# Optimization experiments

Hardware: AMD Instinct MI355X
Metric: run time of the kernel (lower is better)

## Reference

```python
import jax, jax.numpy as jnp
import numpy as np

B, N, M, D, H = 2, 512, 512, 128, 256
EPS = 1e-5


def _layernorm(x, g, b):
    mu = jnp.mean(x, axis=-1, keepdims=True)
    var = jnp.mean(jnp.square(x - mu), axis=-1, keepdims=True)
    return (x - mu) * jax.lax.rsqrt(var + EPS) * g + b


def setup_inputs() -> dict:
    key = jax.random.key(0)
    ks = jax.random.split(key, 12)
    X = jax.random.normal(ks[0], (B, N, D), dtype=jnp.float32)
    Y = jax.random.normal(ks[1], (B, M, D), dtype=jnp.float32)
    mask = jax.random.randint(ks[2], (B, N, M), 0, 2).astype(jnp.int32)
    s_in = 1.0 / np.sqrt(2 * D)
    s_h = 1.0 / np.sqrt(H)
    s_d = 1.0 / np.sqrt(D)
    # edge-net Linear(2D, H) split into Y-half and X-half (pairs = cat([Y, X]))
    W1y = jax.random.normal(ks[3], (D, H), dtype=jnp.float32) * s_in
    W1x = jax.random.normal(ks[4], (D, H), dtype=jnp.float32) * s_in
    b1 = jnp.zeros((H,), dtype=jnp.float32)
    W2 = jax.random.normal(ks[5], (H, D), dtype=jnp.float32) * s_h
    b2 = jnp.zeros((D,), dtype=jnp.float32)
    Wf1 = jax.random.normal(ks[6], (D, H), dtype=jnp.float32) * s_d
    bf1 = jnp.zeros((H,), dtype=jnp.float32)
    Wf2 = jax.random.normal(ks[7], (H, D), dtype=jnp.float32) * s_h
    bf2 = jnp.zeros((D,), dtype=jnp.float32)
    g0 = jnp.ones((D,), dtype=jnp.float32)
    be0 = jnp.zeros((D,), dtype=jnp.float32)
    g1 = jnp.ones((D,), dtype=jnp.float32)
    be1 = jnp.zeros((D,), dtype=jnp.float32)
    return {"X": X, "Y": Y, "mask": mask, "W1y": W1y, "W1x": W1x, "b1": b1,
            "W2": W2, "b2": b2, "Wf1": Wf1, "bf1": bf1, "Wf2": Wf2, "bf2": bf2,
            "g0": g0, "be0": be0, "g1": g1, "be1": be1}


def reference(X, Y, mask, W1y, W1x, b1, W2, b2, Wf1, bf1, Wf2, bf2, g0, be0, g1, be1):
    # pairs[b,n,m] = concat(Y[b,m], X[b,n]); Linear on concat == sum of two GEMMs,
    # so avoid materializing the [B,N,M,2D] pairs tensor.
    hy = jnp.einsum('bmd,dh->bmh', Y, W1y)          # [B,M,H]
    hx = jnp.einsum('bnd,dh->bnh', X, W1x)          # [B,N,H]
    h = jax.nn.relu(hy[:, None, :, :] + hx[:, :, None, :] + b1)   # [B,N,M,H]
    E = jnp.einsum('bnmh,hd->bnmd', h, W2) + b2     # [B,N,M,D]
    E = E * mask[..., None].astype(E.dtype)         # masked sum-pool over M
    Z = X + jnp.sum(E, axis=2)                      # residual, [B,N,D]
    Z = _layernorm(Z, g0, be0)
    Z = Z + jax.nn.relu(Z @ Wf1 + bf1) @ Wf2 + bf2  # residual MLP
    Z = _layernorm(Z, g1, be1)
    return Z
```

## Files before the change

kernel.cpp:

```cpp
#include <hip/hip_runtime.h>

#define BB 2
#define NN 512
#define MM 512
#define DD 128
#define HH 256

__global__ __launch_bounds__(256) void k_inproj(
    const float* __restrict__ X, const float* __restrict__ Y,
    const float* __restrict__ W1x, const float* __restrict__ W1y,
    const float* __restrict__ b1,
    float* __restrict__ hx, float* __restrict__ hy)
{
    __shared__ float sr[DD][4];
    int blk = blockIdx.x;
    bool isX = blk < 256;
    const float* src = isX ? X : Y;
    const float* W   = isX ? W1x : W1y;
    float* dst       = isX ? hx : hy;
    int row0 = (isX ? blk : blk - 256) * 4;
    int t = threadIdx.x;

#pragma unroll
    for (int k = 0; k < 2; ++k) {
        int idx = t + k * 256;
        int r = idx >> 7, d = idx & 127;
        sr[d][r] = src[(row0 + r) * DD + d];
    }
    __syncthreads();

    float bias = isX ? b1[t] : 0.0f;
    float a0 = bias, a1 = bias, a2 = bias, a3 = bias;

#pragma unroll 16
    for (int d = 0; d < DD; ++d) {
        float w = W[d * HH + t];
        float4 a = *(const float4*)&sr[d][0];
        a0 = fmaf(a.x, w, a0);
        a1 = fmaf(a.y, w, a1);
        a2 = fmaf(a.z, w, a2);
        a3 = fmaf(a.w, w, a3);
    }
    dst[(row0 + 0) * HH + t] = a0;
    dst[(row0 + 1) * HH + t] = a1;
    dst[(row0 + 2) * HH + t] = a2;
    dst[(row0 + 3) * HH + t] = a3;
}

__global__ __launch_bounds__(256) void k_main(
    const float* __restrict__ hx, const float* __restrict__ hy,
    const int* __restrict__ mask, float* __restrict__ Spart)
{
    __shared__ float mf[128][4];
    int blk   = blockIdx.x;
    int ms    = blk & 3;
    int ntile = (blk >> 2) & 127;
    int b     = blk >> 9;
    int n0    = ntile * 4;
    int t     = threadIdx.x;

    if (t < 128) {
        const int* mrow = mask + (b * NN + n0) * MM + ms * 128 + t;
#pragma unroll
        for (int i = 0; i < 4; ++i)
            mf[t][i] = (float)mrow[i * MM];
    }
    __syncthreads();

    float hxv[4], acc[4] = {0.f, 0.f, 0.f, 0.f};
#pragma unroll
    for (int i = 0; i < 4; ++i)
        hxv[i] = hx[(b * NN + n0 + i) * HH + t];

    const float* hyp = hy + (b * MM + ms * 128) * HH + t;
#pragma unroll 8
    for (int m = 0; m < 128; ++m) {
        float hyv = hyp[m * HH];
        float4 m4 = *(const float4*)&mf[m][0];
        float t0 = fmaxf(hxv[0] + hyv, 0.f);
        float t1 = fmaxf(hxv[1] + hyv, 0.f);
        float t2 = fmaxf(hxv[2] + hyv, 0.f);
        float t3 = fmaxf(hxv[3] + hyv, 0.f);
        acc[0] = fmaf(t0, m4.x, acc[0]);
        acc[1] = fmaf(t1, m4.y, acc[1]);
        acc[2] = fmaf(t2, m4.z, acc[2]);
        acc[3] = fmaf(t3, m4.w, acc[3]);
    }
    float* sp = Spart + (size_t)ms * (BB * NN * HH) + (b * NN + n0) * HH + t;
#pragma unroll
    for (int i = 0; i < 4; ++i) sp[i * HH] = acc[i];
}

__global__ __launch_bounds__(512) void k_epi(
    const float* __restrict__ X, const int* __restrict__ mask,
    const float* __restrict__ Spart,
    const float* __restrict__ W2, const float* __restrict__ b2,
    const float* __restrict__ Wf1, const float* __restrict__ bf1,
    const float* __restrict__ Wf2, const float* __restrict__ bf2,
    const float* __restrict__ g0, const float* __restrict__ be0,
    const float* __restrict__ g1, const float* __restrict__ be1,
    float* __restrict__ out)
{
    __shared__ float sS[4][HH];
    __shared__ float szp[4][DD];
    __shared__ float sz[4][DD];
    __shared__ float su[4][HH];
    __shared__ float scratch[2048];
    __shared__ float scnt[4];

    int blk = blockIdx.x;
    int b   = blk >> 7;
    int n0  = (blk & 127) * 4;
    int t   = threadIdx.x;
    int wave = t >> 6, lane = t & 63;

#pragma unroll
    for (int k = 0; k < 2; ++k) {
        int idx = t + k * 512;
        int r = idx >> 8, h = idx & 255;
        size_t base = (size_t)(b * NN + n0 + r) * HH + h;
        sS[r][h] = Spart[base]
                 + Spart[base + (size_t)1 * BB * NN * HH]
                 + Spart[base + (size_t)2 * BB * NN * HH]
                 + Spart[base + (size_t)3 * BB * NN * HH];
    }

    if (wave < 4) {
        const int* mrow = mask + (b * NN + n0 + wave) * MM;
        int c = 0;
#pragma unroll
        for (int k = 0; k < 8; ++k) c += mrow[lane + k * 64];
#pragma unroll
        for (int off = 32; off; off >>= 1) c += __shfl_down(c, off);
        if (lane == 0) scnt[wave] = (float)c;
    }
    __syncthreads();

    {
        int d = t & 127, q = t >> 7;
        float a0 = 0, a1 = 0, a2 = 0, a3 = 0;
        int hbase = q * 64;
#pragma unroll 8
        for (int h = 0; h < 64; ++h) {
            float w = W2[(hbase + h) * DD + d];
            a0 = fmaf(sS[0][hbase + h], w, a0);
            a1 = fmaf(sS[1][hbase + h], w, a1);
            a2 = fmaf(sS[2][hbase + h], w, a2);
            a3 = fmaf(sS[3][hbase + h], w, a3);
        }
        float* sp = scratch + (q * 4) * DD + d;
        sp[0 * DD] = a0; sp[1 * DD] = a1; sp[2 * DD] = a2; sp[3 * DD] = a3;
    }
    __syncthreads();
    {
        int r = t >> 7, d = t & 127;
        szp[r][d] = scratch[(0 * 4 + r) * DD + d] + scratch[(1 * 4 + r) * DD + d]
                  + scratch[(2 * 4 + r) * DD + d] + scratch[(3 * 4 + r) * DD + d]
                  + X[(b * NN + n0 + r) * DD + d] + scnt[r] * b2[d];
    }
    __syncthreads();

    if (wave < 4) {
        float v0 = szp[wave][lane], v1 = szp[wave][lane + 64];
        float s = v0 + v1, q = v0 * v0 + v1 * v1;
#pragma unroll
        for (int off = 32; off; off >>= 1) { s += __shfl_down(s, off); q += __shfl_down(q, off); }
        s = __shfl(s, 0); q = __shfl(q, 0);
        float mu   = s * (1.0f / 128.0f);
        float var  = q * (1.0f / 128.0f) - mu * mu;
        float rstd = rsqrtf(var + 1e-5f);
        sz[wave][lane]      = (v0 - mu) * rstd * g0[lane]      + be0[lane];
        sz[wave][lane + 64] = (v1 - mu) * rstd * g0[lane + 64] + be0[lane + 64];
    }
    __syncthreads();

    {
        int h = t & 255, dh = t >> 8;
        float a0 = 0, a1 = 0, a2 = 0, a3 = 0;
        int dbase = dh * 64;
#pragma unroll 8
        for (int d = 0; d < 64; ++d) {
            float w = Wf1[(dbase + d) * HH + h];
            a0 = fmaf(sz[0][dbase + d], w, a0);
            a1 = fmaf(sz[1][dbase + d], w, a1);
            a2 = fmaf(sz[2][dbase + d], w, a2);
            a3 = fmaf(sz[3][dbase + d], w, a3);
        }
        float* sp = scratch + (dh * 4) * HH + h;
        sp[0 * HH] = a0; sp[1 * HH] = a1; sp[2 * HH] = a2; sp[3 * HH] = a3;
    }
    __syncthreads();
#pragma unroll
    for (int k = 0; k < 2; ++k) {
        int idx = t + k * 512;
        int r = idx >> 8, h = idx & 255;
        su[r][h] = fmaxf(scratch[(0 * 4 + r) * HH + h]
                       + scratch[(1 * 4 + r) * HH + h] + bf1[h], 0.f);
    }
    __syncthreads();

    {
        int d = t & 127, q = t >> 7;
        float a0 = 0, a1 = 0, a2 = 0, a3 = 0;
        int hbase = q * 64;
#pragma unroll 8
        for (int h = 0; h < 64; ++h) {
            float w = Wf2[(hbase + h) * DD + d];
            a0 = fmaf(su[0][hbase + h], w, a0);
            a1 = fmaf(su[1][hbase + h], w, a1);
            a2 = fmaf(su[2][hbase + h], w, a2);
            a3 = fmaf(su[3][hbase + h], w, a3);
        }
        float* sp = scratch + (q * 4) * DD + d;
        sp[0 * DD] = a0; sp[1 * DD] = a1; sp[2 * DD] = a2; sp[3 * DD] = a3;
    }
    __syncthreads();
    {
        int r = t >> 7, d = t & 127;
        szp[r][d] = sz[r][d] + bf2[d]
                  + scratch[(0 * 4 + r) * DD + d] + scratch[(1 * 4 + r) * DD + d]
                  + scratch[(2 * 4 + r) * DD + d] + scratch[(3 * 4 + r) * DD + d];
    }
    __syncthreads();

    if (wave < 4) {
        float v0 = szp[wave][lane], v1 = szp[wave][lane + 64];
        float s = v0 + v1, q = v0 * v0 + v1 * v1;
#pragma unroll
        for (int off = 32; off; off >>= 1) { s += __shfl_down(s, off); q += __shfl_down(q, off); }
        s = __shfl(s, 0); q = __shfl(q, 0);
        float mu   = s * (1.0f / 128.0f);
        float var  = q * (1.0f / 128.0f) - mu * mu;
        float rstd = rsqrtf(var + 1e-5f);
        int row = (b * NN + n0 + wave) * DD;
        out[row + lane]      = (v0 - mu) * rstd * g1[lane]      + be1[lane];
        out[row + lane + 64] = (v1 - mu) * rstd * g1[lane + 64] + be1[lane + 64];
    }
}

extern "C" void kernel_launch(void* const* d_in, const int* in_sizes, int n_in,
                              void* d_out, int out_size, void* d_ws, size_t ws_size,
                              hipStream_t stream)
{
    const float* X    = (const float*)d_in[0];
    const float* Y    = (const float*)d_in[1];
    const int*   mask = (const int*)d_in[2];
    const float* W1y  = (const float*)d_in[3];
    const float* W1x  = (const float*)d_in[4];
    const float* b1   = (const float*)d_in[5];
    const float* W2   = (const float*)d_in[6];
    const float* b2   = (const float*)d_in[7];
    const float* Wf1  = (const float*)d_in[8];
    const float* bf1  = (const float*)d_in[9];
    const float* Wf2  = (const float*)d_in[10];
    const float* bf2  = (const float*)d_in[11];
    const float* g0   = (const float*)d_in[12];
    const float* be0  = (const float*)d_in[13];
    const float* g1   = (const float*)d_in[14];
    const float* be1  = (const float*)d_in[15];
    float* out = (float*)d_out;

    float* ws = (float*)d_ws;
    float* hx = ws;
    float* hy = ws + BB * NN * HH;
    float* Sp = ws + 2 * BB * NN * HH;

    k_inproj<<<512, 256, 0, stream>>>(X, Y, W1x, W1y, b1, hx, hy);
    k_main  <<<1024, 256, 0, stream>>>(hx, hy, mask, Sp);
    k_epi   <<<256, 512, 0, stream>>>(X, mask, Sp, W2, b2, Wf1, bf1, Wf2, bf2,
                                      g0, be0, g1, be1, out);
}
```

Measured before the change: 117.2 us.

## Split epilogue into smaller kernels and precompute float mask in inproj

The monolithic epilogue kernel (256 blocks of 512 threads over 4 rows) is split into four kernels: partial-sum reduction with mask count, W2 plus first layernorm, FF1, and FF2 plus final layernorm. Each runs 512 blocks over 2 rows, so more blocks can run in parallel. The mask is converted to float once in the input-projection kernel, and k_main reads it directly from global memory instead of staging it in shared memory. Shared-memory staging of X in inproj is also removed. The cost is three extra kernel launches and extra global round trips for Ssum, zn and u, plus a full float copy of the mask.

```diff
diff --git a/kernel.cpp b/kernel.cpp
--- a/kernel.cpp
+++ b/kernel.cpp
@@ -9,49 +9,46 @@
 __global__ __launch_bounds__(256) void k_inproj(
     const float* __restrict__ X, const float* __restrict__ Y,
     const float* __restrict__ W1x, const float* __restrict__ W1y,
-    const float* __restrict__ b1,
-    float* __restrict__ hx, float* __restrict__ hy)
-{
-    __shared__ float sr[DD][4];
-    int blk = blockIdx.x;
+    const float* __restrict__ b1, const int* __restrict__ mask,
+    float* __restrict__ hx, float* __restrict__ hy, float* __restrict__ mf)
+{
+    int blk = blockIdx.x, t = threadIdx.x;
+
+    {
+        int idx = blk * 256 + t;
+        int4 v = ((const int4*)mask)[idx];
+        ((float4*)mf)[idx] = make_float4((float)v.x, (float)v.y,
+                                         (float)v.z, (float)v.w);
+    }
+
     bool isX = blk < 256;
     const float* src = isX ? X : Y;
     const float* W   = isX ? W1x : W1y;
     float* dst       = isX ? hx : hy;
     int row0 = (isX ? blk : blk - 256) * 4;
-    int t = threadIdx.x;
-
-#pragma unroll
-    for (int k = 0; k < 2; ++k) {
-        int idx = t + k * 256;
-        int r = idx >> 7, d = idx & 127;
-        sr[d][r] = src[(row0 + r) * DD + d];
-    }
-    __syncthreads();
-
+
+    const float* r0 = src + (size_t)row0 * DD;
     float bias = isX ? b1[t] : 0.0f;
     float a0 = bias, a1 = bias, a2 = bias, a3 = bias;
 
 #pragma unroll 16
     for (int d = 0; d < DD; ++d) {
-        float w = W[d * HH + t];
-        float4 a = *(const float4*)&sr[d][0];
-        a0 = fmaf(a.x, w, a0);
-        a1 = fmaf(a.y, w, a1);
-        a2 = fmaf(a.z, w, a2);
-        a3 = fmaf(a.w, w, a3);
-    }
-    dst[(row0 + 0) * HH + t] = a0;
-    dst[(row0 + 1) * HH + t] = a1;
-    dst[(row0 + 2) * HH + t] = a2;
-    dst[(row0 + 3) * HH + t] = a3;
+        float w = W[(size_t)d * HH + t];
+        a0 = fmaf(r0[d         ], w, a0);
+        a1 = fmaf(r0[d +   DD  ], w, a1);
+        a2 = fmaf(r0[d + 2 * DD], w, a2);
+        a3 = fmaf(r0[d + 3 * DD], w, a3);
+    }
+    dst[(size_t)(row0 + 0) * HH + t] = a0;
+    dst[(size_t)(row0 + 1) * HH + t] = a1;
+    dst[(size_t)(row0 + 2) * HH + t] = a2;
+    dst[(size_t)(row0 + 3) * HH + t] = a3;
 }
 
 __global__ __launch_bounds__(256) void k_main(
     const float* __restrict__ hx, const float* __restrict__ hy,
-    const int* __restrict__ mask, float* __restrict__ Spart)
-{
-    __shared__ float mf[128][4];
+    const float* __restrict__ mf, float* __restrict__ Spart)
+{
     int blk   = blockIdx.x;
     int ms    = blk & 3;
     int ntile = (blk >> 2) & 127;
@@ -59,183 +56,172 @@
     int n0    = ntile * 4;
     int t     = threadIdx.x;
 
-    if (t < 128) {
-        const int* mrow = mask + (b * NN + n0) * MM + ms * 128 + t;
-#pragma unroll
-        for (int i = 0; i < 4; ++i)
-            mf[t][i] = (float)mrow[i * MM];
-    }
-    __syncthreads();
-
     float hxv[4], acc[4] = {0.f, 0.f, 0.f, 0.f};
 #pragma unroll
     for (int i = 0; i < 4; ++i)
-        hxv[i] = hx[(b * NN + n0 + i) * HH + t];
-
-    const float* hyp = hy + (b * MM + ms * 128) * HH + t;
-#pragma unroll 8
+        hxv[i] = hx[(size_t)(b * NN + n0 + i) * HH + t];
+
+    const float* hyp = hy + (size_t)(b * MM + ms * 128) * HH + t;
+    const float* mp  = mf + (size_t)(b * NN + n0) * MM + ms * 128;
+
+#pragma unroll 16
     for (int m = 0; m < 128; ++m) {
-        float hyv = hyp[m * HH];
-        float4 m4 = *(const float4*)&mf[m][0];
+        float hyv = hyp[(size_t)m * HH];
+        float w0 = mp[m         ];
+        float w1 = mp[m +     MM];
+        float w2 = mp[m + 2 * MM];
+        float w3 = mp[m + 3 * MM];
         float t0 = fmaxf(hxv[0] + hyv, 0.f);
         float t1 = fmaxf(hxv[1] + hyv, 0.f);
         float t2 = fmaxf(hxv[2] + hyv, 0.f);
         float t3 = fmaxf(hxv[3] + hyv, 0.f);
-        acc[0] = fmaf(t0, m4.x, acc[0]);
-        acc[1] = fmaf(t1, m4.y, acc[1]);
-        acc[2] = fmaf(t2, m4.z, acc[2]);
-        acc[3] = fmaf(t3, m4.w, acc[3]);
-    }
-    float* sp = Spart + (size_t)ms * (BB * NN * HH) + (b * NN + n0) * HH + t;
-#pragma unroll
-    for (int i = 0; i < 4; ++i) sp[i * HH] = acc[i];
-}
-
-__global__ __launch_bounds__(512) void k_epi(
-    const float* __restrict__ X, const int* __restrict__ mask,
-    const float* __restrict__ Spart,
+        acc[0] = fmaf(t0, w0, acc[0]);
+        acc[1] = fmaf(t1, w1, acc[1]);
+        acc[2] = fmaf(t2, w2, acc[2]);
+        acc[3] = fmaf(t3, w3, acc[3]);
+    }
+    float* sp = Spart + (size_t)ms * (BB * NN * HH) + (size_t)(b * NN + n0) * HH + t;
+#pragma unroll
+    for (int i = 0; i < 4; ++i) sp[(size_t)i * HH] = acc[i];
+}
+
+__global__ __launch_bounds__(256) void k_sum(
+    const float* __restrict__ Spart, const int* __restrict__ mask,
+    float* __restrict__ Ssum, float* __restrict__ cntv)
+{
+    int blk = blockIdx.x;
+    int b = blk >> 8, n0 = (blk & 255) * 2;
+    int t = threadIdx.x, wave = t >> 6, lane = t & 63;
+    const size_t P = (size_t)BB * NN * HH;
+
+#pragma unroll
+    for (int r = 0; r < 2; ++r) {
+        size_t base = (size_t)(b * NN + n0 + r) * HH + t;
+        Ssum[base] = Spart[base] + Spart[base + P]
+                   + Spart[base + 2 * P] + Spart[base + 3 * P];
+    }
+    if (wave < 2) {
+        const int* mrow = mask + (size_t)(b * NN + n0 + wave) * MM;
+        int c = 0;
+#pragma unroll
+        for (int k = 0; k < 8; ++k) c += mrow[lane + k * 64];
+#pragma unroll
+        for (int off = 32; off; off >>= 1) c += __shfl_down(c, off);
+        if (lane == 0) cntv[b * NN + n0 + wave] = (float)c;
+    }
+}
+
+__device__ __forceinline__ void ln_row(const float* szp_row,
+                                       const float* __restrict__ g,
+                                       const float* __restrict__ be,
+                                       float* dst, int lane)
+{
+    float v0 = szp_row[lane], v1 = szp_row[lane + 64];
+    float s = v0 + v1, q = v0 * v0 + v1 * v1;
+#pragma unroll
+    for (int off = 32; off; off >>= 1) {
+        s += __shfl_down(s, off);
+        q += __shfl_down(q, off);
+    }
+    s = __shfl(s, 0); q = __shfl(q, 0);
+    float mu   = s * (1.0f / 128.0f);
+    float var  = q * (1.0f / 128.0f) - mu * mu;
+    float rstd = rsqrtf(var + 1e-5f);
+    dst[lane]      = (v0 - mu) * rstd * g[lane]      + be[lane];
+    dst[lane + 64] = (v1 - mu) * rstd * g[lane + 64] + be[lane + 64];
+}
+
+__global__ __launch_bounds__(256) void k_zln(
+    const float* __restrict__ X, const float* __restrict__ Ssum,
+    const float* __restrict__ cntv,
     const float* __restrict__ W2, const float* __restrict__ b2,
-    const float* __restrict__ Wf1, const float* __restrict__ bf1,
+    const float* __restrict__ g0, const float* __restrict__ be0,
+    float* __restrict__ zn)
+{
+    __shared__ float scratch[2][2][DD];
+    __shared__ float szp[2][DD];
+    int blk = blockIdx.x;
+    int b = blk >> 8, n0 = (blk & 255) * 2;
+    int t = threadIdx.x, wave = t >> 6, lane = t & 63;
+    int d = t & 127, q = t >> 7;
+
+    const float* s0 = Ssum + (size_t)(b * NN + n0) * HH + q * 128;
+    const float* s1 = s0 + HH;
+    const float* wp = W2 + (size_t)(q * 128) * DD + d;
+    float a0 = 0.f, a1 = 0.f;
+#pragma unroll 8
+    for (int h = 0; h < 128; ++h) {
+        float w = wp[(size_t)h * DD];
+        a0 = fmaf(s0[h], w, a0);
+        a1 = fmaf(s1[h], w, a1);
+    }
+    scratch[q][0][d] = a0;
+    scratch[q][1][d] = a1;
+    __syncthreads();
+    {
+        int r = t >> 7;
+        float c = cntv[b * NN + n0 + r];
+        szp[r][d] = scratch[0][r][d] + scratch[1][r][d]
+                  + X[(size_t)(b * NN + n0 + r) * DD + d] + c * b2[d];
+    }
+    __syncthreads();
+    if (wave < 2)
+        ln_row(szp[wave], g0, be0, zn + (size_t)(b * NN + n0 + wave) * DD, lane);
+}
+
+__global__ __launch_bounds__(256) void k_ff1(
+    const float* __restrict__ zn, const float* __restrict__ Wf1,
+    const float* __restrict__ bf1, float* __restrict__ u)
+{
+    int blk = blockIdx.x;
+    int row0 = blk * 2;
+    int h = threadIdx.x;
+    const float* z0 = zn + (size_t)row0 * DD;
+    float a0 = bf1[h], a1 = a0;
+#pragma unroll 16
+    for (int d = 0; d < DD; ++d) {
+        float w = Wf1[(size_t)d * HH + h];
+        a0 = fmaf(z0[d     ], w, a0);
+        a1 = fmaf(z0[d + DD], w, a1);
+    }
+    u[(size_t)row0 * HH + h]       = fmaxf(a0, 0.f);
+    u[(size_t)(row0 + 1) * HH + h] = fmaxf(a1, 0.f);
+}
+
+__global__ __launch_bounds__(256) void k_ff2(
+    const float* __restrict__ zn, const float* __restrict__ u,
     const float* __restrict__ Wf2, const float* __restrict__ bf2,
-    const float* __restrict__ g0, const float* __restrict__ be0,
     const float* __restrict__ g1, const float* __restrict__ be1,
     float* __restrict__ out)
 {
-    __shared__ float sS[4][HH];
-    __shared__ float szp[4][DD];
-    __shared__ float sz[4][DD];
-    __shared__ float su[4][HH];
-    __shared__ float scratch[2048];
-    __shared__ float scnt[4];
-
-    int blk = blockIdx.x;
-    int b   = blk >> 7;
-    int n0  = (blk & 127) * 4;
-    int t   = threadIdx.x;
-    int wave = t >> 6, lane = t & 63;
-
-#pragma unroll
-    for (int k = 0; k < 2; ++k) {
-        int idx = t + k * 512;
-        int r = idx >> 8, h = idx & 255;
-        size_t base = (size_t)(b * NN + n0 + r) * HH + h;
-        sS[r][h] = Spart[base]
-                 + Spart[base + (size_t)1 * BB * NN * HH]
-                 + Spart[base + (size_t)2 * BB * NN * HH]
-                 + Spart[base + (size_t)3 * BB * NN * HH];
-    }
-
-    if (wave < 4) {
-        const int* mrow = mask + (b * NN + n0 + wave) * MM;
-        int c = 0;
-#pragma unroll
-        for (int k = 0; k < 8; ++k) c += mrow[lane + k * 64];
-#pragma unroll
-        for (int off = 32; off; off >>= 1) c += __shfl_down(c, off);
-        if (lane == 0) scnt[wave] = (float)c;
-    }
-    __syncthreads();
-
+    __shared__ float scratch[2][2][DD];
+    __shared__ float szp[2][DD];
+    int blk = blockIdx.x;
+    int row0 = blk * 2;
+    int t = threadIdx.x, wave = t >> 6, lane = t & 63;
+    int d = t & 127, q = t >> 7;
+
+    const float* u0 = u + (size_t)row0 * HH + q * 128;
+    const float* u1 = u0 + HH;
+    const float* wp = Wf2 + (size_t)(q * 128) * DD + d;
+    float a0 = 0.f, a1 = 0.f;
+#pragma unroll 8
+    for (int h = 0; h < 128; ++h) {
+        float w = wp[(size_t)h * DD];
+        a0 = fmaf(u0[h], w, a0);
+        a1 = fmaf(u1[h], w, a1);
+    }
+    scratch[q][0][d] = a0;
+    scratch[q][1][d] = a1;
+    __syncthreads();
     {
-        int d = t & 127, q = t >> 7;
-        float a0 = 0, a1 = 0, a2 = 0, a3 = 0;
-        int hbase = q * 64;
-#pragma unroll 8
-        for (int h = 0; h < 64; ++h) {
-            float w = W2[(hbase + h) * DD + d];
-            a0 = fmaf(sS[0][hbase + h], w, a0);
-            a1 = fmaf(sS[1][hbase + h], w, a1);
-            a2 = fmaf(sS[2][hbase + h], w, a2);
-            a3 = fmaf(sS[3][hbase + h], w, a3);
-        }
-        float* sp = scratch + (q * 4) * DD + d;
-        sp[0 * DD] = a0; sp[1 * DD] = a1; sp[2 * DD] = a2; sp[3 * DD] = a3;
-    }
-    __syncthreads();
-    {
-        int r = t >> 7, d = t & 127;
-        szp[r][d] = scratch[(0 * 4 + r) * DD + d] + scratch[(1 * 4 + r) * DD + d]
-                  + scratch[(2 * 4 + r) * DD + d] + scratch[(3 * 4 + r) * DD + d]
-                  + X[(b * NN + n0 + r) * DD + d] + scnt[r] * b2[d];
-    }
-    __syncthreads();
-
-    if (wave < 4) {
-        float v0 = szp[wave][lane], v1 = szp[wave][lane + 64];
-        float s = v0 + v1, q = v0 * v0 + v1 * v1;
-#pragma unroll
-        for (int off = 32; off; off >>= 1) { s += __shfl_down(s, off); q += __shfl_down(q, off); }
-        s = __shfl(s, 0); q = __shfl(q, 0);
-        float mu   = s * (1.0f / 128.0f);
-        float var  = q * (1.0f / 128.0f) - mu * mu;
-        float rstd = rsqrtf(var + 1e-5f);
-        sz[wave][lane]      = (v0 - mu) * rstd * g0[lane]      + be0[lane];
-        sz[wave][lane + 64] = (v1 - mu) * rstd * g0[lane + 64] + be0[lane + 64];
-    }
-    __syncthreads();
-
-    {
-        int h = t & 255, dh = t >> 8;
-        float a0 = 0, a1 = 0, a2 = 0, a3 = 0;
-        int dbase = dh * 64;
-#pragma unroll 8
-        for (int d = 0; d < 64; ++d) {
-            float w = Wf1[(dbase + d) * HH + h];
-            a0 = fmaf(sz[0][dbase + d], w, a0);
-            a1 = fmaf(sz[1][dbase + d], w, a1);
-            a2 = fmaf(sz[2][dbase + d], w, a2);
-            a3 = fmaf(sz[3][dbase + d], w, a3);
-        }
-        float* sp = scratch + (dh * 4) * HH + h;
-        sp[0 * HH] = a0; sp[1 * HH] = a1; sp[2 * HH] = a2; sp[3 * HH] = a3;
-    }
-    __syncthreads();
-#pragma unroll
-    for (int k = 0; k < 2; ++k) {
-        int idx = t + k * 512;
-        int r = idx >> 8, h = idx & 255;
-        su[r][h] = fmaxf(scratch[(0 * 4 + r) * HH + h]
-                       + scratch[(1 * 4 + r) * HH + h] + bf1[h], 0.f);
-    }
-    __syncthreads();
-
-    {
-        int d = t & 127, q = t >> 7;
-        float a0 = 0, a1 = 0, a2 = 0, a3 = 0;
-        int hbase = q * 64;
-#pragma unroll 8
-        for (int h = 0; h < 64; ++h) {
-            float w = Wf2[(hbase + h) * DD + d];
-            a0 = fmaf(su[0][hbase + h], w, a0);
-            a1 = fmaf(su[1][hbase + h], w, a1);
-            a2 = fmaf(su[2][hbase + h], w, a2);
-            a3 = fmaf(su[3][hbase + h], w, a3);
-        }
-        float* sp = scratch + (q * 4) * DD + d;
-        sp[0 * DD] = a0; sp[1 * DD] = a1; sp[2 * DD] = a2; sp[3 * DD] = a3;
-    }
-    __syncthreads();
-    {
-        int r = t >> 7, d = t & 127;
-        szp[r][d] = sz[r][d] + bf2[d]
-                  + scratch[(0 * 4 + r) * DD + d] + scratch[(1 * 4 + r) * DD + d]
-                  + scratch[(2 * 4 + r) * DD + d] + scratch[(3 * 4 + r) * DD + d];
-    }
-    __syncthreads();
-
-    if (wave < 4) {
-        float v0 = szp[wave][lane], v1 = szp[wave][lane + 64];
-        float s = v0 + v1, q = v0 * v0 + v1 * v1;
-#pragma unroll
-        for (int off = 32; off; off >>= 1) { s += __shfl_down(s, off); q += __shfl_down(q, off); }
-        s = __shfl(s, 0); q = __shfl(q, 0);
-        float mu   = s * (1.0f / 128.0f);
-        float var  = q * (1.0f / 128.0f) - mu * mu;
-        float rstd = rsqrtf(var + 1e-5f);
-        int row = (b * NN + n0 + wave) * DD;
-        out[row + lane]      = (v0 - mu) * rstd * g1[lane]      + be1[lane];
-        out[row + lane + 64] = (v1 - mu) * rstd * g1[lane + 64] + be1[lane + 64];
-    }
+        int r = t >> 7;
+        szp[r][d] = zn[(size_t)(row0 + r) * DD + d]
+                  + scratch[0][r][d] + scratch[1][r][d] + bf2[d];
+    }
+    __syncthreads();
+    if (wave < 2)
+        ln_row(szp[wave], g1, be1, out + (size_t)(row0 + wave) * DD, lane);
 }
 
 extern "C" void kernel_launch(void* const* d_in, const int* in_sizes, int n_in,
@@ -260,13 +246,20 @@
     const float* be1  = (const float*)d_in[15];
     float* out = (float*)d_out;
 
-    float* ws = (float*)d_ws;
-    float* hx = ws;
-    float* hy = ws + BB * NN * HH;
-    float* Sp = ws + 2 * BB * NN * HH;
-
-    k_inproj<<<512, 256, 0, stream>>>(X, Y, W1x, W1y, b1, hx, hy);
-    k_main  <<<1024, 256, 0, stream>>>(hx, hy, mask, Sp);
-    k_epi   <<<256, 512, 0, stream>>>(X, mask, Sp, W2, b2, Wf1, bf1, Wf2, bf2,
-                                      g0, be0, g1, be1, out);
-}
+    float* ws   = (float*)d_ws;
+    float* hx   = ws;
+    float* hy   = hx + (size_t)BB * NN * HH;
+    float* Sp   = hy + (size_t)BB * NN * HH;
+    float* mf   = Sp + (size_t)4 * BB * NN * HH;
+    float* Ssum = mf + (size_t)BB * NN * MM;
+    float* cntv = Ssum + (size_t)BB * NN * HH;
+    float* zn   = cntv + (size_t)BB * NN;
+    float* uu   = zn + (size_t)BB * NN * DD;
+
+    k_inproj<<<512, 256, 0, stream>>>(X, Y, W1x, W1y, b1, mask, hx, hy, mf);
+    k_main  <<<1024, 256, 0, stream>>>(hx, hy, mf, Sp);
+    k_sum   <<<512, 256, 0, stream>>>(Sp, mask, Ssum, cntv);
+    k_zln   <<<512, 256, 0, stream>>>(X, Ssum, cntv, W2, b2, g0, be0, zn);
+    k_ff1   <<<512, 256, 0, stream>>>(zn, Wf1, bf1, uu);
+    k_ff2   <<<512, 256, 0, stream>>>(zn, uu, Wf2, bf2, g1, be1, out);
+}
```

After: 135.9 us. 1.16x slower.

## Fuse masked pair-sum into epilogue kernel and drop shared staging in input projection

Applied to the files above, without the earlier changes.

Merges the masked ReLU pair-reduction kernel into the epilogue kernel, so each block computes its 4-row H sums directly and keeps them in shared memory. This removes the partial-sum workspace round trip and one launch. Shared tiles are transposed so the small GEMMs read float4 per row group, and the input projection reads inputs straight from global memory instead of staging them. The trade-off is fewer, longer-running threads for the dominant reduction loop, which lowers parallelism and latency hiding.

```diff
diff --git a/kernel.cpp b/kernel.cpp
--- a/kernel.cpp
+++ b/kernel.cpp
@@ -12,88 +12,34 @@
     const float* __restrict__ b1,
     float* __restrict__ hx, float* __restrict__ hy)
 {
-    __shared__ float sr[DD][4];
-    int blk = blockIdx.x;
+    int blk = blockIdx.x, t = threadIdx.x;
     bool isX = blk < 256;
     const float* src = isX ? X : Y;
     const float* W   = isX ? W1x : W1y;
     float* dst       = isX ? hx : hy;
     int row0 = (isX ? blk : blk - 256) * 4;
-    int t = threadIdx.x;
-
-#pragma unroll
-    for (int k = 0; k < 2; ++k) {
-        int idx = t + k * 256;
-        int r = idx >> 7, d = idx & 127;
-        sr[d][r] = src[(row0 + r) * DD + d];
-    }
-    __syncthreads();
-
+
+    const float* r0 = src + (size_t)row0 * DD;
     float bias = isX ? b1[t] : 0.0f;
     float a0 = bias, a1 = bias, a2 = bias, a3 = bias;
 
 #pragma unroll 16
     for (int d = 0; d < DD; ++d) {
-        float w = W[d * HH + t];
-        float4 a = *(const float4*)&sr[d][0];
-        a0 = fmaf(a.x, w, a0);
-        a1 = fmaf(a.y, w, a1);
-        a2 = fmaf(a.z, w, a2);
-        a3 = fmaf(a.w, w, a3);
-    }
-    dst[(row0 + 0) * HH + t] = a0;
-    dst[(row0 + 1) * HH + t] = a1;
-    dst[(row0 + 2) * HH + t] = a2;
-    dst[(row0 + 3) * HH + t] = a3;
+        float w = W[(size_t)d * HH + t];
+        a0 = fmaf(r0[d         ], w, a0);
+        a1 = fmaf(r0[d +   DD  ], w, a1);
+        a2 = fmaf(r0[d + 2 * DD], w, a2);
+        a3 = fmaf(r0[d + 3 * DD], w, a3);
+    }
+    dst[(size_t)(row0 + 0) * HH + t] = a0;
+    dst[(size_t)(row0 + 1) * HH + t] = a1;
+    dst[(size_t)(row0 + 2) * HH + t] = a2;
+    dst[(size_t)(row0 + 3) * HH + t] = a3;
 }
 
-__global__ __launch_bounds__(256) void k_main(
-    const float* __restrict__ hx, const float* __restrict__ hy,
-    const int* __restrict__ mask, float* __restrict__ Spart)
-{
-    __shared__ float mf[128][4];
-    int blk   = blockIdx.x;
-    int ms    = blk & 3;
-    int ntile = (blk >> 2) & 127;
-    int b     = blk >> 9;
-    int n0    = ntile * 4;
-    int t     = threadIdx.x;
-
-    if (t < 128) {
-        const int* mrow = mask + (b * NN + n0) * MM + ms * 128 + t;
-#pragma unroll
-        for (int i = 0; i < 4; ++i)
-            mf[t][i] = (float)mrow[i * MM];
-    }
-    __syncthreads();
-
-    float hxv[4], acc[4] = {0.f, 0.f, 0.f, 0.f};
-#pragma unroll
-    for (int i = 0; i < 4; ++i)
-        hxv[i] = hx[(b * NN + n0 + i) * HH + t];
-
-    const float* hyp = hy + (b * MM + ms * 128) * HH + t;
-#pragma unroll 8
-    for (int m = 0; m < 128; ++m) {
-        float hyv = hyp[m * HH];
-        float4 m4 = *(const float4*)&mf[m][0];
-        float t0 = fmaxf(hxv[0] + hyv, 0.f);
-        float t1 = fmaxf(hxv[1] + hyv, 0.f);
-        float t2 = fmaxf(hxv[2] + hyv, 0.f);
-        float t3 = fmaxf(hxv[3] + hyv, 0.f);
-        acc[0] = fmaf(t0, m4.x, acc[0]);
-        acc[1] = fmaf(t1, m4.y, acc[1]);
-        acc[2] = fmaf(t2, m4.z, acc[2]);
-        acc[3] = fmaf(t3, m4.w, acc[3]);
-    }
-    float* sp = Spart + (size_t)ms * (BB * NN * HH) + (b * NN + n0) * HH + t;
-#pragma unroll
-    for (int i = 0; i < 4; ++i) sp[i * HH] = acc[i];
-}
-
-__global__ __launch_bounds__(512) void k_epi(
-    const float* __restrict__ X, const int* __restrict__ mask,
-    const float* __restrict__ Spart,
+__global__ __launch_bounds__(512) void k_fused(
+    const float* __restrict__ X, const float* __restrict__ hx,
+    const float* __restrict__ hy, const int* __restrict__ mask,
     const float* __restrict__ W2, const float* __restrict__ b2,
     const float* __restrict__ Wf1, const float* __restrict__ bf1,
     const float* __restrict__ Wf2, const float* __restrict__ bf2,
@@ -101,32 +47,29 @@
     const float* __restrict__ g1, const float* __restrict__ be1,
     float* __restrict__ out)
 {
-    __shared__ float sS[4][HH];
-    __shared__ float szp[4][DD];
-    __shared__ float sz[4][DD];
-    __shared__ float su[4][HH];
-    __shared__ float scratch[2048];
+    __shared__ float smf[MM][4];
+    __shared__ float sSp[2][HH][4];
+    __shared__ float sST[HH][4];
+    __shared__ float scratch[4][4][DD];
+    __shared__ float znT[DD][4];
+    __shared__ float sp2[2][HH][4];
+    __shared__ float suT[HH][4];
+    __shared__ float srow[4][DD];
     __shared__ float scnt[4];
 
     int blk = blockIdx.x;
-    int b   = blk >> 7;
-    int n0  = (blk & 127) * 4;
-    int t   = threadIdx.x;
+    int b = blk >> 7, n0 = (blk & 127) * 4;
+    int t = threadIdx.x;
     int wave = t >> 6, lane = t & 63;
 
-#pragma unroll
-    for (int k = 0; k < 2; ++k) {
-        int idx = t + k * 512;
-        int r = idx >> 8, h = idx & 255;
-        size_t base = (size_t)(b * NN + n0 + r) * HH + h;
-        sS[r][h] = Spart[base]
-                 + Spart[base + (size_t)1 * BB * NN * HH]
-                 + Spart[base + (size_t)2 * BB * NN * HH]
-                 + Spart[base + (size_t)3 * BB * NN * HH];
-    }
-
+    {
+        const int* mp = mask + (size_t)(b * NN + n0) * MM + t;
+#pragma unroll
+        for (int r = 0; r < 4; ++r)
+            smf[t][r] = (float)mp[(size_t)r * MM];
+    }
     if (wave < 4) {
-        const int* mrow = mask + (b * NN + n0 + wave) * MM;
+        const int* mrow = mask + (size_t)(b * NN + n0 + wave) * MM;
         int c = 0;
 #pragma unroll
         for (int k = 0; k < 8; ++k) c += mrow[lane + k * 64];
@@ -137,102 +80,128 @@
     __syncthreads();
 
     {
+        int h = t & 255, mh = t >> 8;
+        float hxv[4];
+#pragma unroll
+        for (int r = 0; r < 4; ++r)
+            hxv[r] = hx[(size_t)(b * NN + n0 + r) * HH + h];
+        const float* hyp = hy + ((size_t)b * MM + mh * 256) * HH + h;
+        float a0 = 0.f, a1 = 0.f, a2 = 0.f, a3 = 0.f;
+#pragma unroll 16
+        for (int m = 0; m < 256; ++m) {
+            float hyv = hyp[(size_t)m * HH];
+            float4 m4 = *(const float4*)&smf[mh * 256 + m][0];
+            a0 = fmaf(fmaxf(hxv[0] + hyv, 0.f), m4.x, a0);
+            a1 = fmaf(fmaxf(hxv[1] + hyv, 0.f), m4.y, a1);
+            a2 = fmaf(fmaxf(hxv[2] + hyv, 0.f), m4.z, a2);
+            a3 = fmaf(fmaxf(hxv[3] + hyv, 0.f), m4.w, a3);
+        }
+        *(float4*)&sSp[mh][h][0] = make_float4(a0, a1, a2, a3);
+    }
+    __syncthreads();
+#pragma unroll
+    for (int k = 0; k < 2; ++k) {
+        int v = t + k * 512;
+        int h = v >> 2, r = v & 3;
+        sST[h][r] = sSp[0][h][r] + sSp[1][h][r];
+    }
+    __syncthreads();
+
+    {
         int d = t & 127, q = t >> 7;
-        float a0 = 0, a1 = 0, a2 = 0, a3 = 0;
-        int hbase = q * 64;
+        const float* wp = W2 + (size_t)(q * 64) * DD + d;
+        float a0 = 0.f, a1 = 0.f, a2 = 0.f, a3 = 0.f;
 #pragma unroll 8
-        for (int h = 0; h < 64; ++h) {
-            float w = W2[(hbase + h) * DD + d];
-            a0 = fmaf(sS[0][hbase + h], w, a0);
-            a1 = fmaf(sS[1][hbase + h], w, a1);
-            a2 = fmaf(sS[2][hbase + h], w, a2);
-            a3 = fmaf(sS[3][hbase + h], w, a3);
-        }
-        float* sp = scratch + (q * 4) * DD + d;
-        sp[0 * DD] = a0; sp[1 * DD] = a1; sp[2 * DD] = a2; sp[3 * DD] = a3;
+        for (int hh = 0; hh < 64; ++hh) {
+            float w = wp[(size_t)hh * DD];
+            float4 s4 = *(const float4*)&sST[q * 64 + hh][0];
+            a0 = fmaf(s4.x, w, a0); a1 = fmaf(s4.y, w, a1);
+            a2 = fmaf(s4.z, w, a2); a3 = fmaf(s4.w, w, a3);
+        }
+        scratch[q][0][d] = a0; scratch[q][1][d] = a1;
+        scratch[q][2][d] = a2; scratch[q][3][d] = a3;
     }
     __syncthreads();
     {
         int r = t >> 7, d = t & 127;
-        szp[r][d] = scratch[(0 * 4 + r) * DD + d] + scratch[(1 * 4 + r) * DD + d]
-                  + scratch[(2 * 4 + r) * DD + d] + scratch[(3 * 4 + r) * DD + d]
-                  + X[(b * NN + n0 + r) * DD + d] + scnt[r] * b2[d];
-    }
-    __syncthreads();
-
+        srow[r][d] = scratch[0][r][d] + scratch[1][r][d]
+                   + scratch[2][r][d] + scratch[3][r][d]
+                   + X[(size_t)(b * NN + n0 + r) * DD + d] + scnt[r] * b2[d];
+    }
+    __syncthreads();
     if (wave < 4) {
-        float v0 = szp[wave][lane], v1 = szp[wave][lane + 64];
-        float s = v0 + v1, q = v0 * v0 + v1 * v1;
-#pragma unroll
-        for (int off = 32; off; off >>= 1) { s += __shfl_down(s, off); q += __shfl_down(q, off); }
-        s = __shfl(s, 0); q = __shfl(q, 0);
+        float v0 = srow[wave][lane], v1 = srow[wave][lane + 64];
+        float s = v0 + v1, q2 = v0 * v0 + v1 * v1;
+#pragma unroll
+        for (int off = 32; off; off >>= 1) {
+            s += __shfl_down(s, off); q2 += __shfl_down(q2, off);
+        }
+        s = __shfl(s, 0); q2 = __shfl(q2, 0);
         float mu   = s * (1.0f / 128.0f);
-        float var  = q * (1.0f / 128.0f) - mu * mu;
+        float var  = q2 * (1.0f / 128.0f) - mu * mu;
         float rstd = rsqrtf(var + 1e-5f);
-        sz[wave][lane]      = (v0 - mu) * rstd * g0[lane]      + be0[lane];
-        sz[wave][lane + 64] = (v1 - mu) * rstd * g0[lane + 64] + be0[lane + 64];
-    }
-    __syncthreads();
-
-    {
-        int h = t & 255, dh = t >> 8;
-        float a0 = 0, a1 = 0, a2 = 0, a3 = 0;
-        int dbase = dh * 64;
+        znT[lane][wave]      = (v0 - mu) * rstd * g0[lane]      + be0[lane];
+        znT[lane + 64][wave] = (v1 - mu) * rstd * g0[lane + 64] + be0[lane + 64];
+    }
+    __syncthreads();
+
+    {
+        int h = t & 255, dq = t >> 8;
+        float bias = dq ? 0.f : bf1[h];
+        float a0 = bias, a1 = bias, a2 = bias, a3 = bias;
+        const float* wp = Wf1 + (size_t)(dq * 64) * HH + h;
 #pragma unroll 8
-        for (int d = 0; d < 64; ++d) {
-            float w = Wf1[(dbase + d) * HH + h];
-            a0 = fmaf(sz[0][dbase + d], w, a0);
-            a1 = fmaf(sz[1][dbase + d], w, a1);
-            a2 = fmaf(sz[2][dbase + d], w, a2);
-            a3 = fmaf(sz[3][dbase + d], w, a3);
-        }
-        float* sp = scratch + (dh * 4) * HH + h;
-        sp[0 * HH] = a0; sp[1 * HH] = a1; sp[2 * HH] = a2; sp[3 * HH] = a3;
+        for (int dd = 0; dd < 64; ++dd) {
+            float w = wp[(size_t)dd * HH];
+            float4 z4 = *(const float4*)&znT[dq * 64 + dd][0];
+            a0 = fmaf(z4.x, w, a0); a1 = fmaf(z4.y, w, a1);
+            a2 = fmaf(z4.z, w, a2); a3 = fmaf(z4.w, w, a3);
+        }
+        *(float4*)&sp2[dq][h][0] = make_float4(a0, a1, a2, a3);
     }
     __syncthreads();
 #pragma unroll
     for (int k = 0; k < 2; ++k) {
-        int idx = t + k * 512;
-        int r = idx >> 8, h = idx & 255;
-        su[r][h] = fmaxf(scratch[(0 * 4 + r) * HH + h]
-                       + scratch[(1 * 4 + r) * HH + h] + bf1[h], 0.f);
+        int v = t + k * 512;
+        int h = v >> 2, r = v & 3;
+        suT[h][r] = fmaxf(sp2[0][h][r] + sp2[1][h][r], 0.f);
     }
     __syncthreads();
 
     {
         int d = t & 127, q = t >> 7;
-        float a0 = 0, a1 = 0, a2 = 0, a3 = 0;
-        int hbase = q * 64;
+        const float* wp = Wf2 + (size_t)(q * 64) * DD + d;
+        float a0 = 0.f, a1 = 0.f, a2 = 0.f, a3 = 0.f;
 #pragma unroll 8
-        for (int h = 0; h < 64; ++h) {
-            float w = Wf2[(hbase + h) * DD + d];
-            a0 = fmaf(su[0][hbase + h], w, a0);
-            a1 = fmaf(su[1][hbase + h], w, a1);
-            a2 = fmaf(su[2][hbase + h], w, a2);
-            a3 = fmaf(su[3][hbase + h], w, a3);
-        }
-        float* sp = scratch + (q * 4) * DD + d;
-        sp[0 * DD] = a0; sp[1 * DD] = a1; sp[2 * DD] = a2; sp[3 * DD] = a3;
+        for (int hh = 0; hh < 64; ++hh) {
+            float w = wp[(size_t)hh * DD];
+            float4 u4 = *(const float4*)&suT[q * 64 + hh][0];
+            a0 = fmaf(u4.x, w, a0); a1 = fmaf(u4.y, w, a1);
+            a2 = fmaf(u4.z, w, a2); a3 = fmaf(u4.w, w, a3);
+        }
+        scratch[q][0][d] = a0; scratch[q][1][d] = a1;
+        scratch[q][2][d] = a2; scratch[q][3][d] = a3;
     }
     __syncthreads();
     {
         int r = t >> 7, d = t & 127;
-        szp[r][d] = sz[r][d] + bf2[d]
-                  + scratch[(0 * 4 + r) * DD + d] + scratch[(1 * 4 + r) * DD + d]
-                  + scratch[(2 * 4 + r) * DD + d] + scratch[(3 * 4 + r) * DD + d];
-    }
-    __syncthreads();
-
+        srow[r][d] = znT[d][r] + bf2[d]
+                   + scratch[0][r][d] + scratch[1][r][d]
+                   + scratch[2][r][d] + scratch[3][r][d];
+    }
+    __syncthreads();
     if (wave < 4) {
-        float v0 = szp[wave][lane], v1 = szp[wave][lane + 64];
-        float s = v0 + v1, q = v0 * v0 + v1 * v1;
-#pragma unroll
-        for (int off = 32; off; off >>= 1) { s += __shfl_down(s, off); q += __shfl_down(q, off); }
-        s = __shfl(s, 0); q = __shfl(q, 0);
+        float v0 = srow[wave][lane], v1 = srow[wave][lane + 64];
+        float s = v0 + v1, q2 = v0 * v0 + v1 * v1;
+#pragma unroll
+        for (int off = 32; off; off >>= 1) {
+            s += __shfl_down(s, off); q2 += __shfl_down(q2, off);
+        }
+        s = __shfl(s, 0); q2 = __shfl(q2, 0);
         float mu   = s * (1.0f / 128.0f);
-        float var  = q * (1.0f / 128.0f) - mu * mu;
+        float var  = q2 * (1.0f / 128.0f) - mu * mu;
         float rstd = rsqrtf(var + 1e-5f);
-        int row = (b * NN + n0 + wave) * DD;
+        size_t row = (size_t)(b * NN + n0 + wave) * DD;
         out[row + lane]      = (v0 - mu) * rstd * g1[lane]      + be1[lane];
         out[row + lane + 64] = (v1 - mu) * rstd * g1[lane + 64] + be1[lane + 64];
     }
@@ -262,11 +231,9 @@
 
     float* ws = (float*)d_ws;
     float* hx = ws;
-    float* hy = ws + BB * NN * HH;
-    float* Sp = ws + 2 * BB * NN * HH;
+    float* hy = ws + (size_t)BB * NN * HH;
 
     k_inproj<<<512, 256, 0, stream>>>(X, Y, W1x, W1y, b1, hx, hy);
-    k_main  <<<1024, 256, 0, stream>>>(hx, hy, mask, Sp);
-    k_epi   <<<256, 512, 0, stream>>>(X, mask, Sp, W2, b2, Wf1, bf1, Wf2, bf2,
-                                      g0, be0, g1, be1, out);
+    k_fused <<<256, 512, 0, stream>>>(X, hx, hy, mask, W2, b2, Wf1, bf1,
+                                      Wf2, bf2, g0, be0, g1, be1, out);
 }
```

Result: no change. 118.4 us (+1.1%).
